# Performance work log

Measured on AMD Instinct MI355X. Metric: run time of the kernel, lower is better.

Reference implementation:

```python
import jax, jax.numpy as jnp
import numpy as np

PERI_IDX = np.array([0, 1, 2, 3, 5, 6, 7, 8])  # non-center taps of the 3x3 window


def _extract_patches(x, stride, padding):
    # x: [B,C,H,W] -> patches [B,C,9,Hout,Wout], tap k = di*3+dj (row-major), matching F.unfold.
    B, C, H, W = x.shape
    Hout = (H + 2 * padding - 3) // stride + 1
    Wout = (W + 2 * padding - 3) // stride + 1
    xp = jnp.pad(x, ((0, 0), (0, 0), (padding, padding), (padding, padding)))
    taps = [xp[:, :, di:di + (Hout - 1) * stride + 1:stride, dj:dj + (Wout - 1) * stride + 1:stride]
            for di in range(3) for dj in range(3)]
    return jnp.stack(taps, axis=2)  # [B,C,9,Hout,Wout]


def setup_inputs() -> dict:
    key = jax.random.key(0)
    k1, k2, k3, k4 = jax.random.split(key, 4)
    B, C, O, H, W = 8, 64, 64, 128, 128
    x = jax.random.normal(k1, (B, C, H, W), dtype=jnp.float32)
    core = jax.random.normal(k2, (O, C, 1, 1), dtype=jnp.float32) * (1.0 / np.sqrt(C))
    periphery = jax.random.uniform(k3, (8,), dtype=jnp.float32, minval=-0.1, maxval=0.1)
    threshold = jnp.array([0.1], dtype=jnp.float32)
    scale = jnp.array([10.0], dtype=jnp.float32)
    return {"x": x, "core": core, "periphery": periphery, "threshold": threshold,
            "scale": scale, "stride": 1, "padding": 1}


def reference(x, core, periphery, threshold, scale, stride, padding):
    B, C, H, W = x.shape
    O = core.shape[0]
    patches = _extract_patches(x, stride, padding)           # [B,C,9,Ho,Wo]
    center = patches[:, :, 4]                                 # [B,C,Ho,Wo]
    # per-pixel variance-like routing statistic over channels and taps
    div = jnp.sum((patches - center[:, :, None]) ** 2, axis=(1, 2))  # [B,Ho,Wo]
    m_hard = jax.nn.sigmoid((div - threshold[0]) * scale[0]) > 0.5   # [B,Ho,Wo] bool
    w = core.reshape(O, C)
    # path 0 (low variance): 1x1 conv on the center pixel
    zero_out = jnp.einsum('bchw,oc->bohw', center, w)
    # path 1 (high variance): periphery-weighted sum then 1x1 conv
    agg = jnp.einsum('bckhw,k->bchw', patches[:, :, PERI_IDX], periphery)
    one_out = jnp.einsum('bchw,oc->bohw', agg, w)
    return jnp.where(m_hard[:, None], one_out, zero_out)
```

## Files before the change

kernel.cpp:

```cpp
#include <hip/hip_runtime.h>
#include <hip/hip_bf16.h>

constexpr int Bc = 8;
constexpr int Cc = 64;
constexpr int Oc = 64;
constexpr int Hc = 128;
constexpr int Wc = 128;
constexpr int HWc = Hc * Wc;
constexpr int CP = 72;

typedef __attribute__((ext_vector_type(8))) short short8;
typedef __attribute__((ext_vector_type(4))) float floatx4;
typedef __attribute__((ext_vector_type(2))) float floatx2;

__device__ __forceinline__ float bperm(int idx4, float v) {
    return __int_as_float(__builtin_amdgcn_ds_bpermute(idx4, __float_as_int(v)));
}
__device__ __forceinline__ unsigned cvt_pk_bf16(float lo, float hi) {
    unsigned r;
    asm("v_cvt_pk_bf16_f32 %0, %1, %2" : "=v"(r) : "v"(lo), "v"(hi));
    return r;
}

__global__ __launch_bounds__(512, 4) void spconv_kernel(
    const float* __restrict__ x, const float* __restrict__ core,
    const float* __restrict__ peri, const float* __restrict__ thr,
    const float* __restrict__ scl, float* __restrict__ out)
{
    __shared__ __hip_bfloat16 s_selT[2][Wc][CP];
    __shared__ __hip_bfloat16 s_core[Oc][CP];
    __shared__ float s_divp[2][8][Wc];
    __shared__ float s_msk[2][Wc];
    __shared__ int   s_any;

    const int tid = threadIdx.x;
    const int l   = tid & 63;
    const int wv  = tid >> 6;
    const int b   = blockIdx.x & 7;
    const int hp  = blockIdx.x >> 3;
    const int h0  = hp * 2;

    if (tid == 0) s_any = 0;

    #pragma unroll
    for (int i = 0; i < 2; ++i) {
        const int idx = (i * 512 + tid) * 4;
        const floatx4 v = *(const floatx4*)(core + idx);
        unsigned* dst = (unsigned*)&s_core[idx >> 6][idx & 63];
        dst[0] = cvt_pk_bf16(v.x, v.y);
        dst[1] = cvt_pk_bf16(v.z, v.w);
    }

    const int upIdx = ((l - 1) & 63) << 2;
    const int dnIdx = ((l + 1) & 63) << 2;
    const float lzf = (l == 0)  ? 0.f : 1.f;
    const float rzf = (l == 63) ? 0.f : 1.f;
    const float mUf = (h0 > 0) ? 1.f : 0.f;
    const float mDf = (h0 < Hc - 2) ? 1.f : 0.f;
    const int   dU  = (h0 > 0) ? -Wc : 0;
    const int   dD2 = (h0 < Hc - 2) ? 2 * Wc : Wc;

    const float p0 = peri[0], p1 = peri[1], p2 = peri[2], p3 = peri[3];
    const float p4 = peri[4], p5 = peri[5], p6 = peri[6], p7 = peri[7];

    const float* xw = x + (size_t)b * Cc * HWc + (size_t)h0 * Wc + 2 * l;
    const float* xb = x + (size_t)b * Cc * HWc + (size_t)h0 * Wc;

    float dAlo = 0.f, dAhi = 0.f, dBlo = 0.f, dBhi = 0.f;

#define PROC(RM, R0, R1, R2, K) do {                                          \
    const float rmL = lzf * bperm(upIdx, RM.y);                               \
    const float r0L = lzf * bperm(upIdx, R0.y);                               \
    const float r1L = lzf * bperm(upIdx, R1.y);                               \
    const float r2L = lzf * bperm(upIdx, R2.y);                               \
    const float rmR = rzf * bperm(dnIdx, RM.x);                               \
    const float r0R = rzf * bperm(dnIdx, R0.x);                               \
    const float r1R = rzf * bperm(dnIdx, R1.x);                               \
    const float r2R = rzf * bperm(dnIdx, R2.x);                               \
    { const float t = R0.x;                       \
      float a = p0 * rmL; a = fmaf(p1, RM.x, a); a = fmaf(p2, RM.y, a);       \
      a = fmaf(p3, r0L, a); a = fmaf(p4, R0.y, a);                            \
      a = fmaf(p5, r1L, a); a = fmaf(p6, R1.x, a); a = fmaf(p7, R1.y, a);     \
      aAlo[K] = a; float e;                                                   \
      e = rmL  - t; dAlo = fmaf(e, e, dAlo); e = RM.x - t; dAlo = fmaf(e, e, dAlo); \
      e = RM.y - t; dAlo = fmaf(e, e, dAlo); e = r0L  - t; dAlo = fmaf(e, e, dAlo); \
      e = R0.y - t; dAlo = fmaf(e, e, dAlo); e = r1L  - t; dAlo = fmaf(e, e, dAlo); \
      e = R1.x - t; dAlo = fmaf(e, e, dAlo); e = R1.y - t; dAlo = fmaf(e, e, dAlo); } \
    { const float t = R0.y;                     \
      float a = p0 * RM.x; a = fmaf(p1, RM.y, a); a = fmaf(p2, rmR, a);       \
      a = fmaf(p3, R0.x, a); a = fmaf(p4, r0R, a);                            \
      a = fmaf(p5, R1.x, a); a = fmaf(p6, R1.y, a); a = fmaf(p7, r1R, a);     \
      aAhi[K] = a; float e;                                                   \
      e = RM.x - t; dAhi = fmaf(e, e, dAhi); e = RM.y - t; dAhi = fmaf(e, e, dAhi); \
      e = rmR  - t; dAhi = fmaf(e, e, dAhi); e = R0.x - t; dAhi = fmaf(e, e, dAhi); \
      e = r0R  - t; dAhi = fmaf(e, e, dAhi); e = R1.x - t; dAhi = fmaf(e, e, dAhi); \
      e = R1.y - t; dAhi = fmaf(e, e, dAhi); e = r1R  - t; dAhi = fmaf(e, e, dAhi); } \
    { const float t = R1.x;                              \
      float a = p0 * r0L; a = fmaf(p1, R0.x, a); a = fmaf(p2, R0.y, a);       \
      a = fmaf(p3, r1L, a); a = fmaf(p4, R1.y, a);                            \
      a = fmaf(p5, r2L, a); a = fmaf(p6, R2.x, a); a = fmaf(p7, R2.y, a);     \
      aBlo[K] = a; float e;                                                   \
      e = r0L  - t; dBlo = fmaf(e, e, dBlo); e = R0.x - t; dBlo = fmaf(e, e, dBlo); \
      e = R0.y - t; dBlo = fmaf(e, e, dBlo); e = r1L  - t; dBlo = fmaf(e, e, dBlo); \
      e = R1.y - t; dBlo = fmaf(e, e, dBlo); e = r2L  - t; dBlo = fmaf(e, e, dBlo); \
      e = R2.x - t; dBlo = fmaf(e, e, dBlo); e = R2.y - t; dBlo = fmaf(e, e, dBlo); } \
    { const float t = R1.y;                              \
      float a = p0 * R0.x; a = fmaf(p1, R0.y, a); a = fmaf(p2, r0R, a);       \
      a = fmaf(p3, R1.x, a); a = fmaf(p4, r1R, a);                            \
      a = fmaf(p5, R2.x, a); a = fmaf(p6, R2.y, a); a = fmaf(p7, r2R, a);     \
      aBhi[K] = a; float e;                                                   \
      e = R0.x - t; dBhi = fmaf(e, e, dBhi); e = R0.y - t; dBhi = fmaf(e, e, dBhi); \
      e = r0R  - t; dBhi = fmaf(e, e, dBhi); e = R1.x - t; dBhi = fmaf(e, e, dBhi); \
      e = r1R  - t; dBhi = fmaf(e, e, dBhi); e = R2.x - t; dBhi = fmaf(e, e, dBhi); \
      e = R2.y - t; dBhi = fmaf(e, e, dBhi); e = r2R  - t; dBhi = fmaf(e, e, dBhi); } \
} while (0)

    #pragma unroll 2
    for (int j = 0; j < 4; ++j) {
        const int c0 = wv * 8 + 2 * j;
        const float* b0p = xw + (size_t)c0 * HWc;
        const float* b1p = b0p + HWc;

        floatx2 rm0 = *(const floatx2*)(b0p + dU);
        floatx2 r00 = *(const floatx2*)(b0p);
        floatx2 r10 = *(const floatx2*)(b0p + Wc);
        floatx2 r20 = *(const floatx2*)(b0p + dD2);
        floatx2 rm1 = *(const floatx2*)(b1p + dU);
        floatx2 r01 = *(const floatx2*)(b1p);
        floatx2 r11 = *(const floatx2*)(b1p + Wc);
        floatx2 r21 = *(const floatx2*)(b1p + dD2);
        rm0 *= mUf; r20 *= mDf; rm1 *= mUf; r21 *= mDf;

        float aAlo[2], aAhi[2], aBlo[2], aBhi[2];
        PROC(rm0, r00, r10, r20, 0);
        PROC(rm1, r01, r11, r21, 1);

        *(unsigned*)&s_selT[0][l]      [c0] = cvt_pk_bf16(aAlo[0], aAlo[1]);
        *(unsigned*)&s_selT[0][64 + l] [c0] = cvt_pk_bf16(aAhi[0], aAhi[1]);
        *(unsigned*)&s_selT[1][l]      [c0] = cvt_pk_bf16(aBlo[0], aBlo[1]);
        *(unsigned*)&s_selT[1][64 + l] [c0] = cvt_pk_bf16(aBhi[0], aBhi[1]);
    }
#undef PROC

    {
        floatx2 da = {dAlo, dAhi}, db = {dBlo, dBhi};
        *(floatx2*)&s_divp[0][wv][2 * l] = da;
        *(floatx2*)&s_divp[1][wv][2 * l] = db;
    }
    __syncthreads();

    const int o0   = (wv & 3) * 16;
    const int wh   = wv >> 2;
    const int n    = l & 15;
    const int quad = l >> 4;
    const short8 a0 = *(const short8*)&s_core[o0 + n][quad * 8];
    const short8 a1 = *(const short8*)&s_core[o0 + n][quad * 8 + 32];

    if (tid < 2 * Wc) {
        const int rr = tid >> 7, ww = tid & (Wc - 1);
        float dv = s_divp[rr][0][ww];
        #pragma unroll
        for (int g = 1; g < 8; ++g) dv += s_divp[rr][g][ww];
        const bool one = ((dv - thr[0]) * scl[0]) > 0.f;
        s_msk[rr][ww] = one ? 1.f : 0.f;
        if (!one) s_any = 1;
    }
    __syncthreads();

    if (s_any) {
        #pragma unroll
        for (int i = 0; i < 32; ++i) {
            const int idx = i * 512 + tid;
            const int rr  = idx >> 13;
            const int e2  = idx & 8191;
            const int p   = e2 & (Wc - 1);
            const int c   = e2 >> 7;
            const int ww  = ((p & 63) << 1) | (p >> 6);
            if (s_msk[rr][ww] == 0.f)
                s_selT[rr][p][c] =
                    __float2bfloat16(xb[(size_t)c * HWc + rr * Wc + ww]);
        }
        __syncthreads();
    }

    float* outb = out + ((size_t)(b * Oc) * Hc + h0) * Wc;

    #pragma unroll
    for (int rr = 0; rr < 2; ++rr) {
        #pragma unroll
        for (int t = 0; t < 4; ++t) {
            const int w0   = (wh * 4 + t) * 16;
            const int wlog = w0 + n;
            const int pr   = ((wlog >> 1) & 63) | ((wlog & 1) << 6);
            const short8 b0 = *(const short8*)&s_selT[rr][pr][quad * 8];
            const short8 b1 = *(const short8*)&s_selT[rr][pr][quad * 8 + 32];
            floatx4 acc = {0.f, 0.f, 0.f, 0.f};
            acc = __builtin_amdgcn_mfma_f32_16x16x32_bf16(a0, b0, acc, 0, 0, 0);
            acc = __builtin_amdgcn_mfma_f32_16x16x32_bf16(a1, b1, acc, 0, 0, 0);
            #pragma unroll
            for (int r = 0; r < 4; ++r) {
                const int o = o0 + quad * 4 + r;
                outb[(size_t)o * HWc + rr * Wc + w0 + n] = acc[r];
            }
        }
    }
}

extern "C" void kernel_launch(void* const* d_in, const int* in_sizes, int n_in,
                              void* d_out, int out_size, void* d_ws, size_t ws_size,
                              hipStream_t stream) {
    const float* x    = (const float*)d_in[0];
    const float* core = (const float*)d_in[1];
    const float* peri = (const float*)d_in[2];
    const float* thr  = (const float*)d_in[3];
    const float* scl  = (const float*)d_in[4];
    float* out = (float*)d_out;

    spconv_kernel<<<dim3(Bc * Hc / 2), dim3(512), 0, stream>>>(
        x, core, peri, thr, scl, out);
}
```

Before: 97.39 us.

## Preload all input rows into registers, keep core weights in VGPRs, drop barrier

All 32 row loads per thread are issued up front into a register array so global memory latency overlaps, instead of loading inside a partially unrolled loop. The weight matrix is read straight into bf16 MFMA operand registers, which removes the shared-memory staging of the core weights. The shared any-flag and its extra barrier are replaced by a per-wave __any reduction that every wave computes identically. The register array holds 64 floats per thread, which under the 512×4 launch bounds risks spills or lower occupancy.

```diff
diff --git a/kernel.cpp b/kernel.cpp
--- a/kernel.cpp
+++ b/kernel.cpp
@@ -28,10 +28,8 @@
     const float* __restrict__ scl, float* __restrict__ out)
 {
     __shared__ __hip_bfloat16 s_selT[2][Wc][CP];
-    __shared__ __hip_bfloat16 s_core[Oc][CP];
     __shared__ float s_divp[2][8][Wc];
     __shared__ float s_msk[2][Wc];
-    __shared__ int   s_any;
 
     const int tid = threadIdx.x;
     const int l   = tid & 63;
@@ -40,16 +38,42 @@
     const int hp  = blockIdx.x >> 3;
     const int h0  = hp * 2;
 
-    if (tid == 0) s_any = 0;
-
-    #pragma unroll
-    for (int i = 0; i < 2; ++i) {
-        const int idx = (i * 512 + tid) * 4;
-        const floatx4 v = *(const floatx4*)(core + idx);
-        unsigned* dst = (unsigned*)&s_core[idx >> 6][idx & 63];
-        dst[0] = cvt_pk_bf16(v.x, v.y);
-        dst[1] = cvt_pk_bf16(v.z, v.w);
-    }
+    const int o0   = (wv & 3) * 16;
+    const int wh   = wv >> 2;
+    const int n    = l & 15;
+    const int quad = l >> 4;
+
+    const float* arow = core + (size_t)(o0 + n) * Cc + quad * 8;
+    const floatx4 af0 = *(const floatx4*)(arow);
+    const floatx4 af1 = *(const floatx4*)(arow + 4);
+    const floatx4 af2 = *(const floatx4*)(arow + 32);
+    const floatx4 af3 = *(const floatx4*)(arow + 36);
+
+    const int   dU  = (h0 > 0) ? -Wc : 0;
+    const int   dD2 = (h0 < Hc - 2) ? 2 * Wc : Wc;
+    const float* xw = x + (size_t)b * Cc * HWc + (size_t)h0 * Wc + 2 * l;
+    const float* xb = x + (size_t)b * Cc * HWc + (size_t)h0 * Wc;
+
+    floatx2 R[4][8];
+    #pragma unroll
+    for (int j = 0; j < 4; ++j) {
+        const float* b0p = xw + (size_t)(wv * 8 + 2 * j) * HWc;
+        const float* b1p = b0p + HWc;
+        R[j][0] = *(const floatx2*)(b0p + dU);
+        R[j][1] = *(const floatx2*)(b0p);
+        R[j][2] = *(const floatx2*)(b0p + Wc);
+        R[j][3] = *(const floatx2*)(b0p + dD2);
+        R[j][4] = *(const floatx2*)(b1p + dU);
+        R[j][5] = *(const floatx2*)(b1p);
+        R[j][6] = *(const floatx2*)(b1p + Wc);
+        R[j][7] = *(const floatx2*)(b1p + dD2);
+    }
+
+    union { unsigned u[4]; short8 s; } A0, A1;
+    A0.u[0] = cvt_pk_bf16(af0.x, af0.y); A0.u[1] = cvt_pk_bf16(af0.z, af0.w);
+    A0.u[2] = cvt_pk_bf16(af1.x, af1.y); A0.u[3] = cvt_pk_bf16(af1.z, af1.w);
+    A1.u[0] = cvt_pk_bf16(af2.x, af2.y); A1.u[1] = cvt_pk_bf16(af2.z, af2.w);
+    A1.u[2] = cvt_pk_bf16(af3.x, af3.y); A1.u[3] = cvt_pk_bf16(af3.z, af3.w);
 
     const int upIdx = ((l - 1) & 63) << 2;
     const int dnIdx = ((l + 1) & 63) << 2;
@@ -57,14 +81,10 @@
     const float rzf = (l == 63) ? 0.f : 1.f;
     const float mUf = (h0 > 0) ? 1.f : 0.f;
     const float mDf = (h0 < Hc - 2) ? 1.f : 0.f;
-    const int   dU  = (h0 > 0) ? -Wc : 0;
-    const int   dD2 = (h0 < Hc - 2) ? 2 * Wc : Wc;
 
     const float p0 = peri[0], p1 = peri[1], p2 = peri[2], p3 = peri[3];
     const float p4 = peri[4], p5 = peri[5], p6 = peri[6], p7 = peri[7];
-
-    const float* xw = x + (size_t)b * Cc * HWc + (size_t)h0 * Wc + 2 * l;
-    const float* xb = x + (size_t)b * Cc * HWc + (size_t)h0 * Wc;
+    const float thrv = thr[0], sclv = scl[0];
 
     float dAlo = 0.f, dAhi = 0.f, dBlo = 0.f, dBhi = 0.f;
 
@@ -115,21 +135,17 @@
       e = R2.y - t; dBhi = fmaf(e, e, dBhi); e = r2R  - t; dBhi = fmaf(e, e, dBhi); } \
 } while (0)
 
-    #pragma unroll 2
+    #pragma unroll
     for (int j = 0; j < 4; ++j) {
         const int c0 = wv * 8 + 2 * j;
-        const float* b0p = xw + (size_t)c0 * HWc;
-        const float* b1p = b0p + HWc;
-
-        floatx2 rm0 = *(const floatx2*)(b0p + dU);
-        floatx2 r00 = *(const floatx2*)(b0p);
-        floatx2 r10 = *(const floatx2*)(b0p + Wc);
-        floatx2 r20 = *(const floatx2*)(b0p + dD2);
-        floatx2 rm1 = *(const floatx2*)(b1p + dU);
-        floatx2 r01 = *(const floatx2*)(b1p);
-        floatx2 r11 = *(const floatx2*)(b1p + Wc);
-        floatx2 r21 = *(const floatx2*)(b1p + dD2);
-        rm0 *= mUf; r20 *= mDf; rm1 *= mUf; r21 *= mDf;
+        floatx2 rm0 = R[j][0] * mUf;
+        floatx2 r00 = R[j][1];
+        floatx2 r10 = R[j][2];
+        floatx2 r20 = R[j][3] * mDf;
+        floatx2 rm1 = R[j][4] * mUf;
+        floatx2 r01 = R[j][5];
+        floatx2 r11 = R[j][6];
+        floatx2 r21 = R[j][7] * mDf;
 
         float aAlo[2], aAhi[2], aBlo[2], aBhi[2];
         PROC(rm0, r00, r10, r20, 0);
@@ -149,25 +165,25 @@
     }
     __syncthreads();
 
-    const int o0   = (wv & 3) * 16;
-    const int wh   = wv >> 2;
-    const int n    = l & 15;
-    const int quad = l >> 4;
-    const short8 a0 = *(const short8*)&s_core[o0 + n][quad * 8];
-    const short8 a1 = *(const short8*)&s_core[o0 + n][quad * 8 + 32];
-
-    if (tid < 2 * Wc) {
-        const int rr = tid >> 7, ww = tid & (Wc - 1);
+    bool bad = false;
+    #pragma unroll
+    for (int k = 0; k < 4; ++k) {
+        const int idx = k * 64 + l;
+        const int rr = idx >> 7, ww = idx & (Wc - 1);
         float dv = s_divp[rr][0][ww];
         #pragma unroll
         for (int g = 1; g < 8; ++g) dv += s_divp[rr][g][ww];
-        const bool one = ((dv - thr[0]) * scl[0]) > 0.f;
-        s_msk[rr][ww] = one ? 1.f : 0.f;
-        if (!one) s_any = 1;
-    }
-    __syncthreads();
-
-    if (s_any) {
+        bad |= (((dv - thrv) * sclv) <= 0.f);
+    }
+    if (__any(bad)) {
+        if (tid < 2 * Wc) {
+            const int rr = tid >> 7, ww = tid & (Wc - 1);
+            float dv = s_divp[rr][0][ww];
+            #pragma unroll
+            for (int g = 1; g < 8; ++g) dv += s_divp[rr][g][ww];
+            s_msk[rr][ww] = (((dv - thrv) * sclv) > 0.f) ? 1.f : 0.f;
+        }
+        __syncthreads();
         #pragma unroll
         for (int i = 0; i < 32; ++i) {
             const int idx = i * 512 + tid;
@@ -195,8 +211,8 @@
             const short8 b0 = *(const short8*)&s_selT[rr][pr][quad * 8];
             const short8 b1 = *(const short8*)&s_selT[rr][pr][quad * 8 + 32];
             floatx4 acc = {0.f, 0.f, 0.f, 0.f};
-            acc = __builtin_amdgcn_mfma_f32_16x16x32_bf16(a0, b0, acc, 0, 0, 0);
-            acc = __builtin_amdgcn_mfma_f32_16x16x32_bf16(a1, b1, acc, 0, 0, 0);
+            acc = __builtin_amdgcn_mfma_f32_16x16x32_bf16(A0.s, b0, acc, 0, 0, 0);
+            acc = __builtin_amdgcn_mfma_f32_16x16x32_bf16(A1.s, b1, acc, 0, 0, 0);
             #pragma unroll
             for (int r = 0; r < 4; ++r) {
                 const int o = o0 + quad * 4 + r;
```

After: 99.28 us. About the same (+1.9%).
